# Performance work log

Measured on AMD Instinct MI355X. Metric: run time of the kernel, lower is better.

Reference implementation:

```python
import jax, jax.numpy as jnp
import numpy as np

BATCH, SEQ = 1, 2048
D_MODEL, N_HEADS, D_HEAD = 2048, 16, 128
ROTARY_DIM = 128
N_CTX = 2048
EPS = 1e-5
IGNORE = -100000.0
ATTN_SCALE = float(np.sqrt(D_HEAD))  # use_attn_scale=True, no layer-idx scaling
ROTARY_BASE = 10000.0


def _ln_pre(x):
    # LayerNormPre: center and normalize, no learned scale/bias
    x = x - x.mean(axis=-1, keepdims=True)
    scale = jnp.sqrt((x * x).mean(axis=-1, keepdims=True) + EPS)
    return x / scale


def _sin_cos_rotary(rotary_dim, n_ctx, base=ROTARY_BASE):
    pos = jnp.arange(n_ctx, dtype=jnp.float32)
    dim = jnp.arange(rotary_dim // 2, dtype=jnp.float32)
    freq = base ** (dim / (rotary_dim / 2))
    freq = jnp.repeat(freq, 2)  # einops.repeat 'd -> (d 2)' (interleaved)
    angles = pos[:, None] / freq[None, :]  # [n_ctx, rotary_dim]
    return jnp.sin(angles), jnp.cos(angles)


def _rotate_every_two(x):
    x1 = x[..., 0::2]
    x2 = x[..., 1::2]
    return jnp.stack([-x2, x1], axis=-1).reshape(x.shape)


def _apply_rotary(x, sin, cos):
    # x: [batch, pos, head, d_head]
    n_pos = x.shape[1]
    x_rot = x[..., :ROTARY_DIM]
    x_pass = x[..., ROTARY_DIM:]
    c = cos[:n_pos][:, None, :]  # [pos, 1, rotary_dim] broadcasts over head
    s = sin[:n_pos][:, None, :]
    x_rotated = x_rot * c + _rotate_every_two(x_rot) * s
    return jnp.concatenate([x_rotated, x_pass], axis=-1)


def setup_inputs() -> dict:
    key = jax.random.key(0)
    ks = jax.random.split(key, 6)
    init_std = 0.02
    return {
        "resid_pre": jax.random.normal(ks[0], (BATCH, SEQ, D_MODEL), jnp.float32),
        "W_Q": jax.random.normal(ks[1], (N_HEADS, D_MODEL, D_HEAD), jnp.float32) * init_std,
        "W_K": jax.random.normal(ks[2], (N_HEADS, D_MODEL, D_HEAD), jnp.float32) * init_std,
        "W_V": jax.random.normal(ks[3], (N_HEADS, D_MODEL, D_HEAD), jnp.float32) * init_std,
        "W_O": jax.random.normal(ks[4], (N_HEADS, D_HEAD, D_MODEL), jnp.float32) * init_std,
        "b_Q": jnp.zeros((N_HEADS, D_HEAD), jnp.float32),
        "b_K": jnp.zeros((N_HEADS, D_HEAD), jnp.float32),
        "b_V": jnp.zeros((N_HEADS, D_HEAD), jnp.float32),
        "b_O": jnp.zeros((D_MODEL,), jnp.float32),
    }


def reference(resid_pre, W_Q, W_K, W_V, W_O, b_Q, b_K, b_V, b_O):
    sin, cos = _sin_cos_rotary(ROTARY_DIM, N_CTX)
    xn = _ln_pre(resid_pre)  # LayerNormPre applied to resid_pre for q, k, v
    q = jnp.einsum("bpd,hde->bphe", xn, W_Q) + b_Q
    k = jnp.einsum("bpd,hde->bphe", xn, W_K) + b_K
    v = jnp.einsum("bpd,hde->bphe", xn, W_V) + b_V
    q = _apply_rotary(q, sin, cos)
    k = _apply_rotary(k, sin, cos)
    # attn_scores: [batch, head, query_pos, key_pos]
    scores = jnp.einsum("bqhe,bkhe->bhqk", q, k) / ATTN_SCALE
    n_pos = resid_pre.shape[1]
    causal = jnp.tril(jnp.ones((n_pos, n_pos), dtype=bool))
    scores = jnp.where(causal, scores, jnp.float32(IGNORE))
    attn = jax.nn.softmax(scores, axis=-1)
    z = jnp.einsum("bkhe,bhqk->bqhe", v, attn)
    out = jnp.einsum("bqhe,hed->bqd", z, W_O) + b_O
    return out
```

## Files before the change

### kernel.cpp

```cpp
#include <hip/hip_runtime.h>
#include <hip/hip_bf16.h>

#define SEQ    2048
#define DM     2048
#define NH     16
#define DH     128
#define EPS    1e-5f
#define SCALE_INV 0.08838834764831845f
#define SC2LOG    0.12751744995f

typedef unsigned short u16;
typedef u16  u16x4  __attribute__((ext_vector_type(4)));
typedef u16  u16x8  __attribute__((ext_vector_type(8)));
typedef unsigned u32x4 __attribute__((ext_vector_type(4)));
typedef __bf16 bf16x8 __attribute__((ext_vector_type(8)));
typedef float f32x4 __attribute__((ext_vector_type(4)));

__device__ __forceinline__ u16 f2bf(float f) {
    unsigned int u = __builtin_bit_cast(unsigned int, f);
    u += 0x7fffu + ((u >> 16) & 1u);
    return (u16)(u >> 16);
}
__device__ __forceinline__ float bf2f(u16 v) {
    return __builtin_bit_cast(float, (unsigned)v << 16);
}
__device__ __forceinline__ bf16x8 as_bf(u16x8 v) { return __builtin_bit_cast(bf16x8, v); }

__device__ __forceinline__ void gload16(const u16* g, u16* l) {
    __builtin_amdgcn_global_load_lds(
        (const __attribute__((address_space(1))) unsigned int*)g,
        (__attribute__((address_space(3))) unsigned int*)l, 16, 0, 0);
}

#define VMCNT(N) asm volatile("s_waitcnt vmcnt(" #N ")" ::: "memory")
#define LGKMCNT0 asm volatile("s_waitcnt lgkmcnt(0)" ::: "memory")
#define SCHEDBAR __builtin_amdgcn_sched_barrier(0)
#define BARRIER  __builtin_amdgcn_s_barrier()

__global__ __launch_bounds__(256) void ln_kernel(const float* __restrict__ x,
                                                 u16* __restrict__ xn,
                                                 float2* __restrict__ rope) {
    int row = blockIdx.x, t = threadIdx.x;
    if (t < 64) {
        float freq = powf(10000.f, (float)t * (1.f / 64.f));
        float ang = (float)row / freq;
        rope[row * 64 + t] = make_float2(sinf(ang), cosf(ang));
    }
    const float* xr = x + (size_t)row * DM;
    float4 v0 = *(const float4*)(xr + t * 4);
    float4 v1 = *(const float4*)(xr + 1024 + t * 4);
    float s = v0.x + v0.y + v0.z + v0.w + v1.x + v1.y + v1.z + v1.w;
    float q = v0.x*v0.x + v0.y*v0.y + v0.z*v0.z + v0.w*v0.w
            + v1.x*v1.x + v1.y*v1.y + v1.z*v1.z + v1.w*v1.w;
    #pragma unroll
    for (int o = 32; o; o >>= 1) { s += __shfl_xor(s, o); q += __shfl_xor(q, o); }
    __shared__ float ss[4], qq[4];
    if ((t & 63) == 0) { ss[t >> 6] = s; qq[t >> 6] = q; }
    __syncthreads();
    s = ss[0] + ss[1] + ss[2] + ss[3];
    q = qq[0] + qq[1] + qq[2] + qq[3];
    float mean = s * (1.f / DM);
    float var  = q * (1.f / DM) - mean * mean;
    float rstd = rsqrtf(var + EPS);
    u16* orow = xn + (size_t)row * DM;
    u16x4 o0 = { f2bf((v0.x-mean)*rstd), f2bf((v0.y-mean)*rstd),
                 f2bf((v0.z-mean)*rstd), f2bf((v0.w-mean)*rstd) };
    u16x4 o1 = { f2bf((v1.x-mean)*rstd), f2bf((v1.y-mean)*rstd),
                 f2bf((v1.z-mean)*rstd), f2bf((v1.w-mean)*rstd) };
    *(u16x4*)(orow + t * 4) = o0;
    *(u16x4*)(orow + 1024 + t * 4) = o1;
}

__global__ __launch_bounds__(256) void transpose_all(const float* __restrict__ WQ,
                                                     const float* __restrict__ WK,
                                                     const float* __restrict__ WV,
                                                     const float* __restrict__ WO,
                                                     u16* __restrict__ outW,
                                                     u16* __restrict__ outWO) {
    int z = blockIdx.z;
    const float* in;
    u16* o;
    int r0 = blockIdx.y * 64, c0;
    int inC, outC;
    if (z < 48) {
        int which = z >> 4, h = z & 15;
        in = ((which == 0) ? WQ : (which == 1) ? WK : WV) + (size_t)h * DM * DH;
        o  = outW + (size_t)z * DM * DH;
        c0 = blockIdx.x * 64;
        inC = DH; outC = DM;
    } else {
        in = WO; o = outWO;
        c0 = ((z - 48) * 2 + blockIdx.x) * 64;
        inC = DM; outC = DM;
    }
    __shared__ u16 tile[64][65];
    int t = threadIdx.x;
    #pragma unroll
    for (int it = 0; it < 4; ++it) {
        int idx = t + it * 256;
        int rr = idx >> 4, cc = (idx & 15) * 4;
        float4 v = *(const float4*)(in + (size_t)(r0 + rr) * inC + c0 + cc);
        tile[rr][cc+0] = f2bf(v.x); tile[rr][cc+1] = f2bf(v.y);
        tile[rr][cc+2] = f2bf(v.z); tile[rr][cc+3] = f2bf(v.w);
    }
    __syncthreads();
    #pragma unroll
    for (int it = 0; it < 4; ++it) {
        int idx = t + it * 256;
        int oc = idx >> 4, orr = (idx & 15) * 4;
        u16x4 w = { tile[orr+0][oc], tile[orr+1][oc], tile[orr+2][oc], tile[orr+3][oc] };
        *(u16x4*)(o + (size_t)(c0 + oc) * outC + r0 + orr) = w;
    }
}

__global__ __launch_bounds__(512, 2) void gemm_qkv(const u16* __restrict__ Xn,
                                                   const u16* __restrict__ Wt,
                                                   const float* __restrict__ bQ,
                                                   const float* __restrict__ bK,
                                                   const float* __restrict__ bV,
                                                   const float2* __restrict__ rope,
                                                   u16* __restrict__ qkv) {
    __shared__ u16 As[2][256 * 64], Bs[2][192 * 64];
    int id = blockIdx.x;
    int swz = (id & 7) * 32 + (id >> 3);
    int bx = swz & 7, by = swz >> 3;
    int m0 = bx * 256, n0 = by * 192;

    int t = threadIdx.x, lane = t & 63, wid = t >> 6;
    int wr = wid >> 2, wc = wid & 3;
    int cl = lane & 15, g = lane >> 4;

    auto stage = [&](int buf, int kt) {
        const u16* xa = Xn + (size_t)kt * 64;
        const u16* xb = Wt + (size_t)kt * 64;
        #pragma unroll
        for (int j = 0; j < 4; ++j) {
            int idx = t + j * 512;
            int row = idx >> 3;
            int slotS = (idx & 7) ^ (row & 7);
            gload16(xa + (size_t)(m0 + row) * DM + slotS * 8, &As[buf][idx * 8]);
        }
        #pragma unroll
        for (int j = 0; j < 3; ++j) {
            int idx = t + j * 512;
            int row = idx >> 3;
            int slotS = (idx & 7) ^ (row & 7);
            gload16(xb + (size_t)(n0 + row) * DM + slotS * 8, &Bs[buf][idx * 8]);
        }
    };

    f32x4 acc[8][3] = {};
    stage(0, 0);
    VMCNT(0);
    BARRIER;

    for (int kt = 0; kt < 32; ++kt) {
        int p = kt & 1;
        bool more = (kt + 1 < 32);
        bf16x8 bfr[3][2], af[4][2];
        #pragma unroll
        for (int nj = 0; nj < 3; ++nj)
            #pragma unroll
            for (int kk = 0; kk < 2; ++kk) {
                int row = wc * 48 + nj * 16 + cl;
                int s = (kk * 4 + g) ^ (row & 7);
                bfr[nj][kk] = as_bf(*(const u16x8*)&Bs[p][row * 64 + s * 8]);
            }
        #pragma unroll
        for (int mi = 0; mi < 4; ++mi)
            #pragma unroll
            for (int kk = 0; kk < 2; ++kk) {
                int row = wr * 128 + mi * 16 + cl;
                int s = (kk * 4 + g) ^ (row & 7);
                af[mi][kk] = as_bf(*(const u16x8*)&As[p][row * 64 + s * 8]);
            }
        if (more) stage(p ^ 1, kt + 1);
        __builtin_amdgcn_s_setprio(1);
        #pragma unroll
        for (int mi = 0; mi < 4; ++mi)
            #pragma unroll
            for (int nj = 0; nj < 3; ++nj)
                #pragma unroll
                for (int kk = 0; kk < 2; ++kk)
                    acc[mi][nj] = __builtin_amdgcn_mfma_f32_16x16x32_bf16(af[mi][kk], bfr[nj][kk], acc[mi][nj], 0, 0, 0);
        __builtin_amdgcn_s_setprio(0);
        #pragma unroll
        for (int mi = 0; mi < 4; ++mi)
            #pragma unroll
            for (int kk = 0; kk < 2; ++kk) {
                int row = wr * 128 + 64 + mi * 16 + cl;
                int s = (kk * 4 + g) ^ (row & 7);
                af[mi][kk] = as_bf(*(const u16x8*)&As[p][row * 64 + s * 8]);
            }
        __builtin_amdgcn_s_setprio(1);
        #pragma unroll
        for (int mi = 0; mi < 4; ++mi)
            #pragma unroll
            for (int nj = 0; nj < 3; ++nj)
                #pragma unroll
                for (int kk = 0; kk < 2; ++kk)
                    acc[4 + mi][nj] = __builtin_amdgcn_mfma_f32_16x16x32_bf16(af[mi][kk], bfr[nj][kk], acc[4 + mi][nj], 0, 0, 0);
        __builtin_amdgcn_s_setprio(0);
        VMCNT(0);
        SCHEDBAR;
        BARRIER;
    }

    #pragma unroll
    for (int i = 0; i < 8; ++i)
        #pragma unroll
        for (int nj = 0; nj < 3; ++nj) {
            int eg = n0 + wc * 48 + nj * 16 + cl;
            int which = eg >> 11;
            int h = (eg >> 7) & 15;
            int e = eg & 127;
            const float* bias = (which == 0) ? bQ : (which == 1) ? bK : bV;
            float bb = bias[h * DH + e];
            int p0 = m0 + wr * 128 + i * 16 + g * 4;
            if (which == 2) {
                u16* vbase = qkv + 2ll * NH * SEQ * DH + (size_t)h * DH * SEQ;
                u16x4 o = { f2bf(acc[i][nj][0] + bb), f2bf(acc[i][nj][1] + bb),
                            f2bf(acc[i][nj][2] + bb), f2bf(acc[i][nj][3] + bb) };
                *(u16x4*)(vbase + (size_t)e * SEQ + p0) = o;
            } else {
                u16* outbase = qkv + ((size_t)which * 16 + h) * SEQ * DH;
                #pragma unroll
                for (int r = 0; r < 4; ++r) {
                    int pp = p0 + r;
                    float v = acc[i][nj][r] + bb;
                    float pv = __shfl_xor(v, 1);
                    float2 sc2 = rope[pp * 64 + (e >> 1)];
                    v = (e & 1) ? (v * sc2.y + pv * sc2.x) : (v * sc2.y - pv * sc2.x);
                    outbase[(size_t)pp * DH + e] = f2bf(v);
                }
            }
        }
}

__device__ __forceinline__ int part_prefix(int j) {
    return (j < 16) ? 2 * (j - 8) : (j < 24 ? 16 + 3 * (j - 16) : 40 + 4 * (j - 24));
}

__global__ __launch_bounds__(256) void flash_kernel(const u16* __restrict__ Qg,
                                                    const u16* __restrict__ Kg,
                                                    const u16* __restrict__ Vt,
                                                    u16* __restrict__ Zg,
                                                    u16* __restrict__ pO,
                                                    float2* __restrict__ ml) {
    __shared__ u16 kt[64 * 128];
    __shared__ u16 vt[128 * 64];
    int h = blockIdx.x;
    int rem = blockIdx.y;
    int j = 31, c = 0;
    #pragma unroll 1
    for (int jj = 31; jj >= 0; --jj) {
        int ncj = (jj >> 3) + 1;
        if (rem < ncj) { j = jj; c = rem; break; }
        rem -= ncj;
    }
    int q0 = j * 64;
    int nc = (j >> 3) + 1;
    bool multi = (nc > 1);
    int kt0 = c * 8;
    int kt1 = min(j, c * 8 + 7);

    int t = threadIdx.x, lane = t & 63, w = t >> 6;
    int cl = lane & 15, g = lane >> 4;
    int qw0 = q0 + w * 16;
    const size_t hs = (size_t)h * SEQ;
    int src0 = cl + ((g & 1) << 5);
    int src1 = src0 + 16;
    bool hi = ((g >> 1) & 1) != 0;

    bf16x8 qf[4];
    #pragma unroll
    for (int st = 0; st < 4; ++st)
        qf[st] = as_bf(*(const u16x8*)(Qg + (hs + qw0 + cl) * DH + st * 32 + g * 8));

    f32x4 acc[8] = {};
    float mrun = -3e38f, lsum = 0.f;

    u16x8 kreg[4], vreg[4];
    auto load_tile = [&](int kv0) {
        #pragma unroll
        for (int jj = 0; jj < 4; ++jj) {
            int idx = t + jj * 256;
            kreg[jj] = *(const u16x8*)(Kg + (hs + kv0 + (idx >> 4)) * DH + (idx & 15) * 8);
            vreg[jj] = *(const u16x8*)(Vt + ((size_t)h * DH + (idx >> 3)) * SEQ + kv0 + (idx & 7) * 8);
        }
    };
    auto store_tile = [&]() {
        #pragma unroll
        for (int jj = 0; jj < 4; ++jj) {
            int idx = t + jj * 256;
            int row = idx >> 4, slot = idx & 15;
            *(u16x8*)((char*)kt + row * 256 + ((slot ^ (row & 7)) * 16)) = kreg[jj];
            int e = idx >> 3, ch = idx & 7;
            *(u16x8*)((char*)vt + e * 128 + ((ch ^ (e & 7)) * 16)) = vreg[jj];
        }
    };

    int kvbeg = kt0 * 64, kvend = kt1 * 64;
    load_tile(kvbeg);
    store_tile();

    for (int kv0 = kvbeg; kv0 <= kvend; kv0 += 64) {
        __syncthreads();
        bool more = (kv0 + 64 <= kvend);
        if (more) load_tile(kv0 + 64);

        f32x4 sc[4] = {};
        __builtin_amdgcn_s_setprio(1);
        #pragma unroll
        for (int st = 0; st < 4; ++st)
            #pragma unroll
            for (int cc = 0; cc < 4; ++cc) {
                int row = cc * 16 + cl;
                bf16x8 kf = as_bf(*(const u16x8*)((char*)kt + row * 256 + (((st * 4 + g) ^ (row & 7)) * 16)));
                sc[cc] = __builtin_amdgcn_mfma_f32_16x16x32_bf16(kf, qf[st], sc[cc], 0, 0, 0);
            }
        __builtin_amdgcn_s_setprio(0);

        bool needmask = (kv0 + 63 > qw0);
        int qrow = qw0 + cl;
        float pf[4][4];
        float tm = -3e38f;
        #pragma unroll
        for (int cc = 0; cc < 4; ++cc)
            #pragma unroll
            for (int r = 0; r < 4; ++r) {
                int kvq = kv0 + cc * 16 + g * 4 + r;
                float sval = sc[cc][r] * SC2LOG;
                if (needmask) sval = (kvq <= qrow) ? sval : -3e38f;
                pf[cc][r] = sval;
                tm = fmaxf(tm, sval);
            }
        tm = fmaxf(tm, __shfl_xor(tm, 16));
        tm = fmaxf(tm, __shfl_xor(tm, 32));

        if (!__all(tm <= mrun + 12.f)) {
            float mn = fmaxf(mrun, tm);
            float alpha = exp2f(mrun - mn);
            mrun = mn;
            lsum *= alpha;
            float aR[4];
            #pragma unroll
            for (int r = 0; r < 4; ++r) aR[r] = __shfl(alpha, g * 4 + r);
            #pragma unroll
            for (int n = 0; n < 8; ++n)
                #pragma unroll
                for (int r = 0; r < 4; ++r) acc[n][r] *= aR[r];
        }
        float rs = 0.f;
        #pragma unroll
        for (int cc = 0; cc < 4; ++cc)
            #pragma unroll
            for (int r = 0; r < 4; ++r) {
                float e2 = exp2f(pf[cc][r] - mrun);
                pf[cc][r] = e2;
                rs += e2;
            }
        rs += __shfl_xor(rs, 16);
        rs += __shfl_xor(rs, 32);
        lsum += rs;

        unsigned U[4][2];
        #pragma unroll
        for (int cc = 0; cc < 4; ++cc) {
            asm("v_cvt_pk_bf16_f32 %0, %1, %2" : "=v"(U[cc][0]) : "v"(pf[cc][0]), "v"(pf[cc][1]));
            asm("v_cvt_pk_bf16_f32 %0, %1, %2" : "=v"(U[cc][1]) : "v"(pf[cc][2]), "v"(pf[cc][3]));
        }
        unsigned wv[2][4];
        #pragma unroll
        for (int ks = 0; ks < 2; ++ks)
            #pragma unroll
            for (int hh = 0; hh < 2; ++hh) {
                unsigned e0 = (unsigned)__shfl((int)U[2*ks][hh],   src0);
                unsigned e1 = (unsigned)__shfl((int)U[2*ks][hh],   src1);
                unsigned o0 = (unsigned)__shfl((int)U[2*ks+1][hh], src0);
                unsigned o1 = (unsigned)__shfl((int)U[2*ks+1][hh], src1);
                wv[ks][hh]     = hi ? o0 : e0;
                wv[ks][2 + hh] = hi ? o1 : e1;
            }
        bf16x8 pa[2];
        {
            u32x4 w0 = { wv[0][0], wv[0][1], wv[0][2], wv[0][3] };
            u32x4 w1 = { wv[1][0], wv[1][1], wv[1][2], wv[1][3] };
            pa[0] = __builtin_bit_cast(bf16x8, w0);
            pa[1] = __builtin_bit_cast(bf16x8, w1);
        }

        __builtin_amdgcn_s_setprio(1);
        #pragma unroll
        for (int n = 0; n < 8; ++n)
            #pragma unroll
            for (int ks = 0; ks < 2; ++ks) {
                int e = n * 16 + cl;
                bf16x8 vf = as_bf(*(const u16x8*)((char*)vt + e * 128 + (((ks * 4 + g) ^ (e & 7)) * 16)));
                acc[n] = __builtin_amdgcn_mfma_f32_16x16x32_bf16(pa[ks], vf, acc[n], 0, 0, 0);
            }
        __builtin_amdgcn_s_setprio(0);

        if (!more) break;
        __syncthreads();
        store_tile();
    }

    if (multi) {
        int pidx = h * 72 + part_prefix(j) + c;
        if (lane < 16) ml[(size_t)pidx * 64 + w * 16 + cl] = make_float2(mrun, lsum);
        u16* po = pO + (size_t)pidx * (64 * 128);
        #pragma unroll
        for (int n = 0; n < 8; ++n)
            #pragma unroll
            for (int r = 0; r < 4; ++r)
                po[(w * 16 + g * 4 + r) * 128 + n * 16 + cl] = f2bf(acc[n][r]);
    } else {
        float inv = 1.0f / lsum;
        float invR[4];
        #pragma unroll
        for (int r = 0; r < 4; ++r) invR[r] = __shfl(inv, g * 4 + r);
        #pragma unroll
        for (int n = 0; n < 8; ++n)
            #pragma unroll
            for (int r = 0; r < 4; ++r) {
                int q = qw0 + g * 4 + r;
                Zg[(hs + q) * DH + n * 16 + cl] = f2bf(acc[n][r] * invR[r]);
            }
    }
}

__global__ __launch_bounds__(256) void merge_kernel(const u16* __restrict__ pO,
                                                    const float2* __restrict__ ml,
                                                    u16* __restrict__ Zg) {
    int h = blockIdx.x;
    int j = blockIdx.y + 8;
    int nc = (j >> 3) + 1;
    int pbase = h * 72 + part_prefix(j);
    int t = threadIdx.x;
    int row = t >> 2;
    int c0 = (t & 3) * 32;

    float mv[4], lv[4];
    float M = -3e38f;
    #pragma unroll
    for (int i = 0; i < 4; ++i) {
        int ii = (i < nc) ? i : 0;
        float2 mli = ml[(size_t)(pbase + ii) * 64 + row];
        mv[i] = mli.x; lv[i] = mli.y;
        if (i < nc) M = fmaxf(M, mli.x);
    }
    float wgt[4];
    float L = 0.f;
    #pragma unroll
    for (int i = 0; i < 4; ++i) {
        wgt[i] = (i < nc) ? exp2f(mv[i] - M) : 0.f;
        L += wgt[i] * lv[i];
    }
    float invL = 1.f / L;

    #pragma unroll
    for (int ccc = 0; ccc < 32; ccc += 8) {
        float o[8] = {};
        #pragma unroll
        for (int i = 0; i < 4; ++i) {
            int ii = (i < nc) ? i : 0;
            u16x8 v = *(const u16x8*)(pO + ((size_t)(pbase + ii) * 64 + row) * 128 + c0 + ccc);
            #pragma unroll
            for (int k = 0; k < 8; ++k) o[k] += wgt[i] * bf2f(v[k]);
        }
        u16x8 zv;
        #pragma unroll
        for (int k = 0; k < 8; ++k) zv[k] = f2bf(o[k] * invL);
        *(u16x8*)(Zg + ((size_t)h * SEQ + j * 64 + row) * DH + c0 + ccc) = zv;
    }
}

__global__ __launch_bounds__(256, 2) void gemm_out(const u16* __restrict__ Z,
                                                   const u16* __restrict__ Wot,
                                                   const float* __restrict__ bO,
                                                   float* __restrict__ out) {
    __shared__ u16 As[2][128 * 64], Bs[2][128 * 64];
    int id = blockIdx.x;
    int swz = (id & 7) * 32 + (id >> 3);
    int m0 = (swz & 15) * 128, n0 = (swz >> 4) * 128;
    int t = threadIdx.x, lane = t & 63, w = t >> 6;
    int wr = w >> 1, wc = w & 1;
    int cl = lane & 15, g = lane >> 4;

    auto stage = [&](int buf, int kt) {
        int k0 = kt * 64;
        int hh = k0 >> 7, e0 = k0 & 127;
        #pragma unroll
        for (int j = 0; j < 4; ++j) {
            int idx = t + j * 256;
            int row = idx >> 3;
            int slotS = (idx & 7) ^ (row & 7);
            gload16(Z + ((size_t)hh * SEQ + m0 + row) * DH + e0 + slotS * 8, &As[buf][idx * 8]);
            gload16(Wot + (size_t)(n0 + row) * DM + k0 + slotS * 8, &Bs[buf][idx * 8]);
        }
    };

    f32x4 acc[4][4] = {};
    stage(0, 0);
    VMCNT(0);
    BARRIER;
    for (int kt = 0; kt < 32; ++kt) {
        int p = kt & 1;
        bool more = (kt + 1 < 32);
        bf16x8 af[4][2], bfr[4][2];
        #pragma unroll
        for (int i = 0; i < 4; ++i)
            #pragma unroll
            for (int kk = 0; kk < 2; ++kk) {
                int rowA = wr * 64 + i * 16 + cl;
                af[i][kk] = as_bf(*(const u16x8*)&As[p][rowA * 64 + (((kk * 4 + g) ^ (rowA & 7)) * 8)]);
                int rowB = wc * 64 + i * 16 + cl;
                bfr[i][kk] = as_bf(*(const u16x8*)&Bs[p][rowB * 64 + (((kk * 4 + g) ^ (rowB & 7)) * 8)]);
            }
        if (more) stage(p ^ 1, kt + 1);
        __builtin_amdgcn_s_setprio(1);
        #pragma unroll
        for (int i = 0; i < 4; ++i)
            #pragma unroll
            for (int j = 0; j < 4; ++j)
                #pragma unroll
                for (int kk = 0; kk < 2; ++kk)
                    acc[i][j] = __builtin_amdgcn_mfma_f32_16x16x32_bf16(af[i][kk], bfr[j][kk], acc[i][j], 0, 0, 0);
        __builtin_amdgcn_s_setprio(0);
        VMCNT(0);
        SCHEDBAR;
        BARRIER;
    }
    #pragma unroll
    for (int i = 0; i < 4; ++i)
        #pragma unroll
        for (int j = 0; j < 4; ++j) {
            int col = n0 + wc * 64 + j * 16 + cl;
            float bb = bO[col];
            #pragma unroll
            for (int r = 0; r < 4; ++r) {
                int p = m0 + wr * 64 + i * 16 + g * 4 + r;
                out[(size_t)p * DM + col] = acc[i][j][r] + bb;
            }
        }
}

extern "C" void kernel_launch(void* const* d_in, const int* in_sizes, int n_in,
                              void* d_out, int out_size, void* d_ws, size_t ws_size,
                              hipStream_t stream) {
    const float* resid = (const float*)d_in[0];
    const float* WQ = (const float*)d_in[1];
    const float* WK = (const float*)d_in[2];
    const float* WV = (const float*)d_in[3];
    const float* WO = (const float*)d_in[4];
    const float* bQ = (const float*)d_in[5];
    const float* bK = (const float*)d_in[6];
    const float* bV = (const float*)d_in[7];
    const float* bO = (const float*)d_in[8];
    float* out = (float*)d_out;
    char* ws = (char*)d_ws;

    float2* rope = (float2*)(ws);
    u16* xn   = (u16*)(ws + (1ll  << 20));
    u16* Wt   = (u16*)(ws + (9ll  << 20));
    u16* Wot  = (u16*)(ws + (33ll << 20));
    u16* qkv  = (u16*)(ws + (41ll << 20));
    u16* z    = (u16*)(ws + (65ll << 20));
    u16* pO   = (u16*)(ws);
    float2* ml = (float2*)(ws + (20ll << 20));

    ln_kernel<<<SEQ, 256, 0, stream>>>(resid, xn, rope);

    transpose_all<<<dim3(2, 32, 64), 256, 0, stream>>>(WQ, WK, WV, WO, Wt, Wot);

    gemm_qkv<<<256, 512, 0, stream>>>(xn, Wt, bQ, bK, bV, rope, qkv);

    const u16* Qg = qkv;
    const u16* Kg = qkv + 1ll * NH * SEQ * DH;
    const u16* Vt = qkv + 2ll * NH * SEQ * DH;
    flash_kernel<<<dim3(NH, 80), 256, 0, stream>>>(Qg, Kg, Vt, z, pO, ml);
    merge_kernel<<<dim3(NH, 24), 256, 0, stream>>>(pO, ml, z);

    gemm_out<<<256, 256, 0, stream>>>(z, Wot, bO, out);
}
```

Baseline: 178.6 us.

## Load K and V fragments directly from global memory in flash kernel

Removes the shared-memory staging of K and V tiles, along with the register prefetch and both block barriers. Each wave now reads its MFMA operand fragments straight from global memory (relying on L1/L2) instead of cooperatively loading and swizzling tiles into LDS. This removes synchronisation and LDS traffic. In exchange, the four waves in a block each fetch the same K/V data redundantly and the loads are no longer prefetched ahead of compute, so memory latency may be exposed.

```diff
diff --git a/kernel.cpp b/kernel.cpp
--- a/kernel.cpp
+++ b/kernel.cpp
@@ -247,8 +247,6 @@
                                                     u16* __restrict__ Zg,
                                                     u16* __restrict__ pO,
                                                     float2* __restrict__ ml) {
-    __shared__ u16 kt[64 * 128];
-    __shared__ u16 vt[128 * 64];
     int h = blockIdx.x;
     int rem = blockIdx.y;
     int j = 31, c = 0;
@@ -272,6 +270,9 @@
     int src1 = src0 + 16;
     bool hi = ((g >> 1) & 1) != 0;
 
+    const u16* kp = Kg + (hs + cl) * DH + g * 8;
+    const u16* vp = Vt + ((size_t)h * DH + cl) * SEQ + g * 8;
+
     bf16x8 qf[4];
     #pragma unroll
     for (int st = 0; st < 4; ++st)
@@ -280,43 +281,16 @@
     f32x4 acc[8] = {};
     float mrun = -3e38f, lsum = 0.f;
 
-    u16x8 kreg[4], vreg[4];
-    auto load_tile = [&](int kv0) {
-        #pragma unroll
-        for (int jj = 0; jj < 4; ++jj) {
-            int idx = t + jj * 256;
-            kreg[jj] = *(const u16x8*)(Kg + (hs + kv0 + (idx >> 4)) * DH + (idx & 15) * 8);
-            vreg[jj] = *(const u16x8*)(Vt + ((size_t)h * DH + (idx >> 3)) * SEQ + kv0 + (idx & 7) * 8);
-        }
-    };
-    auto store_tile = [&]() {
-        #pragma unroll
-        for (int jj = 0; jj < 4; ++jj) {
-            int idx = t + jj * 256;
-            int row = idx >> 4, slot = idx & 15;
-            *(u16x8*)((char*)kt + row * 256 + ((slot ^ (row & 7)) * 16)) = kreg[jj];
-            int e = idx >> 3, ch = idx & 7;
-            *(u16x8*)((char*)vt + e * 128 + ((ch ^ (e & 7)) * 16)) = vreg[jj];
-        }
-    };
-
     int kvbeg = kt0 * 64, kvend = kt1 * 64;
-    load_tile(kvbeg);
-    store_tile();
 
     for (int kv0 = kvbeg; kv0 <= kvend; kv0 += 64) {
-        __syncthreads();
-        bool more = (kv0 + 64 <= kvend);
-        if (more) load_tile(kv0 + 64);
-
         f32x4 sc[4] = {};
         __builtin_amdgcn_s_setprio(1);
         #pragma unroll
         for (int st = 0; st < 4; ++st)
             #pragma unroll
             for (int cc = 0; cc < 4; ++cc) {
-                int row = cc * 16 + cl;
-                bf16x8 kf = as_bf(*(const u16x8*)((char*)kt + row * 256 + (((st * 4 + g) ^ (row & 7)) * 16)));
+                bf16x8 kf = as_bf(*(const u16x8*)(kp + (size_t)(kv0 + cc * 16) * DH + st * 32));
                 sc[cc] = __builtin_amdgcn_mfma_f32_16x16x32_bf16(kf, qf[st], sc[cc], 0, 0, 0);
             }
         __builtin_amdgcn_s_setprio(0);
@@ -395,15 +369,10 @@
         for (int n = 0; n < 8; ++n)
             #pragma unroll
             for (int ks = 0; ks < 2; ++ks) {
-                int e = n * 16 + cl;
-                bf16x8 vf = as_bf(*(const u16x8*)((char*)vt + e * 128 + (((ks * 4 + g) ^ (e & 7)) * 16)));
+                bf16x8 vf = as_bf(*(const u16x8*)(vp + (size_t)(n * 16) * SEQ + kv0 + ks * 32));
                 acc[n] = __builtin_amdgcn_mfma_f32_16x16x32_bf16(pa[ks], vf, acc[n], 0, 0, 0);
             }
         __builtin_amdgcn_s_setprio(0);
-
-        if (!more) break;
-        __syncthreads();
-        store_tile();
     }
 
     if (multi) {
```

Result: slower. 284.5 us (+59.3%).

## Process two 64-row query blocks per flash workgroup to reuse K/V tiles

Applied to the files above, without the earlier changes.

Each flash-attention workgroup now handles 128 query rows, two 16-row strips per wave, against the same shared-memory K/V tiles. This halves the global loads and LDS staging per query row and gives each wave twice the MFMA work between barriers. The partition bookkeeping and the merge kernel are rescaled to match. In exchange the grid shrinks from 1280 to 640 workgroups, register pressure roughly doubles, and more masked work is done on diagonal tiles.

```diff
diff --git a/kernel.cpp b/kernel.cpp
--- a/kernel.cpp
+++ b/kernel.cpp
@@ -238,7 +238,7 @@
 }
 
 __device__ __forceinline__ int part_prefix(int j) {
-    return (j < 16) ? 2 * (j - 8) : (j < 24 ? 16 + 3 * (j - 16) : 40 + 4 * (j - 24));
+    return (j < 8) ? 2 * (j - 4) : (j < 12 ? 8 + 3 * (j - 8) : 20 + 4 * (j - 12));
 }
 
 __global__ __launch_bounds__(256) void flash_kernel(const u16* __restrict__ Qg,
@@ -251,34 +251,38 @@
     __shared__ u16 vt[128 * 64];
     int h = blockIdx.x;
     int rem = blockIdx.y;
-    int j = 31, c = 0;
+    int j = 15, c = 0;
     #pragma unroll 1
-    for (int jj = 31; jj >= 0; --jj) {
-        int ncj = (jj >> 3) + 1;
+    for (int jj = 15; jj >= 0; --jj) {
+        int ncj = (jj >> 2) + 1;
         if (rem < ncj) { j = jj; c = rem; break; }
         rem -= ncj;
     }
-    int q0 = j * 64;
-    int nc = (j >> 3) + 1;
+    int q0 = j * 128;
+    int nc = (j >> 2) + 1;
     bool multi = (nc > 1);
     int kt0 = c * 8;
-    int kt1 = min(j, c * 8 + 7);
+    int kt1 = min(2 * j + 1, c * 8 + 7);
 
     int t = threadIdx.x, lane = t & 63, w = t >> 6;
     int cl = lane & 15, g = lane >> 4;
-    int qw0 = q0 + w * 16;
+    int qs0 = q0 + w * 16;
+    int qs1 = qs0 + 64;
     const size_t hs = (size_t)h * SEQ;
     int src0 = cl + ((g & 1) << 5);
     int src1 = src0 + 16;
     bool hi = ((g >> 1) & 1) != 0;
 
-    bf16x8 qf[4];
-    #pragma unroll
-    for (int st = 0; st < 4; ++st)
-        qf[st] = as_bf(*(const u16x8*)(Qg + (hs + qw0 + cl) * DH + st * 32 + g * 8));
-
-    f32x4 acc[8] = {};
-    float mrun = -3e38f, lsum = 0.f;
+    bf16x8 qf0[4], qf1[4];
+    #pragma unroll
+    for (int st = 0; st < 4; ++st) {
+        qf0[st] = as_bf(*(const u16x8*)(Qg + (hs + qs0 + cl) * DH + st * 32 + g * 8));
+        qf1[st] = as_bf(*(const u16x8*)(Qg + (hs + qs1 + cl) * DH + st * 32 + g * 8));
+    }
+
+    f32x4 acc0[8] = {}, acc1[8] = {};
+    float mrun0 = -3e38f, lsum0 = 0.f;
+    float mrun1 = -3e38f, lsum1 = 0.f;
 
     u16x8 kreg[4], vreg[4];
     auto load_tile = [&](int kv0) {
@@ -309,7 +313,7 @@
         bool more = (kv0 + 64 <= kvend);
         if (more) load_tile(kv0 + 64);
 
-        f32x4 sc[4] = {};
+        f32x4 sc0[4] = {}, sc1[4] = {};
         __builtin_amdgcn_s_setprio(1);
         #pragma unroll
         for (int st = 0; st < 4; ++st)
@@ -317,78 +321,82 @@
             for (int cc = 0; cc < 4; ++cc) {
                 int row = cc * 16 + cl;
                 bf16x8 kf = as_bf(*(const u16x8*)((char*)kt + row * 256 + (((st * 4 + g) ^ (row & 7)) * 16)));
-                sc[cc] = __builtin_amdgcn_mfma_f32_16x16x32_bf16(kf, qf[st], sc[cc], 0, 0, 0);
+                sc0[cc] = __builtin_amdgcn_mfma_f32_16x16x32_bf16(kf, qf0[st], sc0[cc], 0, 0, 0);
+                sc1[cc] = __builtin_amdgcn_mfma_f32_16x16x32_bf16(kf, qf1[st], sc1[cc], 0, 0, 0);
             }
         __builtin_amdgcn_s_setprio(0);
 
-        bool needmask = (kv0 + 63 > qw0);
-        int qrow = qw0 + cl;
-        float pf[4][4];
-        float tm = -3e38f;
-        #pragma unroll
-        for (int cc = 0; cc < 4; ++cc)
-            #pragma unroll
-            for (int r = 0; r < 4; ++r) {
-                int kvq = kv0 + cc * 16 + g * 4 + r;
-                float sval = sc[cc][r] * SC2LOG;
-                if (needmask) sval = (kvq <= qrow) ? sval : -3e38f;
-                pf[cc][r] = sval;
-                tm = fmaxf(tm, sval);
-            }
-        tm = fmaxf(tm, __shfl_xor(tm, 16));
-        tm = fmaxf(tm, __shfl_xor(tm, 32));
-
-        if (!__all(tm <= mrun + 12.f)) {
-            float mn = fmaxf(mrun, tm);
-            float alpha = exp2f(mrun - mn);
-            mrun = mn;
-            lsum *= alpha;
-            float aR[4];
-            #pragma unroll
-            for (int r = 0; r < 4; ++r) aR[r] = __shfl(alpha, g * 4 + r);
-            #pragma unroll
-            for (int n = 0; n < 8; ++n)
-                #pragma unroll
-                for (int r = 0; r < 4; ++r) acc[n][r] *= aR[r];
-        }
-        float rs = 0.f;
-        #pragma unroll
-        for (int cc = 0; cc < 4; ++cc)
-            #pragma unroll
-            for (int r = 0; r < 4; ++r) {
-                float e2 = exp2f(pf[cc][r] - mrun);
-                pf[cc][r] = e2;
-                rs += e2;
-            }
-        rs += __shfl_xor(rs, 16);
-        rs += __shfl_xor(rs, 32);
-        lsum += rs;
-
-        unsigned U[4][2];
-        #pragma unroll
-        for (int cc = 0; cc < 4; ++cc) {
-            asm("v_cvt_pk_bf16_f32 %0, %1, %2" : "=v"(U[cc][0]) : "v"(pf[cc][0]), "v"(pf[cc][1]));
-            asm("v_cvt_pk_bf16_f32 %0, %1, %2" : "=v"(U[cc][1]) : "v"(pf[cc][2]), "v"(pf[cc][3]));
-        }
-        unsigned wv[2][4];
-        #pragma unroll
-        for (int ks = 0; ks < 2; ++ks)
-            #pragma unroll
-            for (int hh = 0; hh < 2; ++hh) {
-                unsigned e0 = (unsigned)__shfl((int)U[2*ks][hh],   src0);
-                unsigned e1 = (unsigned)__shfl((int)U[2*ks][hh],   src1);
-                unsigned o0 = (unsigned)__shfl((int)U[2*ks+1][hh], src0);
-                unsigned o1 = (unsigned)__shfl((int)U[2*ks+1][hh], src1);
-                wv[ks][hh]     = hi ? o0 : e0;
-                wv[ks][2 + hh] = hi ? o1 : e1;
-            }
-        bf16x8 pa[2];
-        {
+        bf16x8 pa0[2], pa1[2];
+        auto smT = [&](f32x4 (&sc)[4], int qb, float& mrun, float& lsum,
+                       f32x4 (&acc)[8], bf16x8 (&pa)[2]) {
+            bool needmask = (kv0 + 63 > qb);
+            int qrow = qb + cl;
+            float pf[4][4];
+            float tm = -3e38f;
+            #pragma unroll
+            for (int cc = 0; cc < 4; ++cc)
+                #pragma unroll
+                for (int r = 0; r < 4; ++r) {
+                    int kvq = kv0 + cc * 16 + g * 4 + r;
+                    float sval = sc[cc][r] * SC2LOG;
+                    if (needmask) sval = (kvq <= qrow) ? sval : -3e38f;
+                    pf[cc][r] = sval;
+                    tm = fmaxf(tm, sval);
+                }
+            tm = fmaxf(tm, __shfl_xor(tm, 16));
+            tm = fmaxf(tm, __shfl_xor(tm, 32));
+
+            if (!__all(tm <= mrun + 12.f)) {
+                float mn = fmaxf(mrun, tm);
+                float alpha = exp2f(mrun - mn);
+                mrun = mn;
+                lsum *= alpha;
+                float aR[4];
+                #pragma unroll
+                for (int r = 0; r < 4; ++r) aR[r] = __shfl(alpha, g * 4 + r);
+                #pragma unroll
+                for (int n = 0; n < 8; ++n)
+                    #pragma unroll
+                    for (int r = 0; r < 4; ++r) acc[n][r] *= aR[r];
+            }
+            float rs = 0.f;
+            #pragma unroll
+            for (int cc = 0; cc < 4; ++cc)
+                #pragma unroll
+                for (int r = 0; r < 4; ++r) {
+                    float e2 = exp2f(pf[cc][r] - mrun);
+                    pf[cc][r] = e2;
+                    rs += e2;
+                }
+            rs += __shfl_xor(rs, 16);
+            rs += __shfl_xor(rs, 32);
+            lsum += rs;
+
+            unsigned U[4][2];
+            #pragma unroll
+            for (int cc = 0; cc < 4; ++cc) {
+                asm("v_cvt_pk_bf16_f32 %0, %1, %2" : "=v"(U[cc][0]) : "v"(pf[cc][0]), "v"(pf[cc][1]));
+                asm("v_cvt_pk_bf16_f32 %0, %1, %2" : "=v"(U[cc][1]) : "v"(pf[cc][2]), "v"(pf[cc][3]));
+            }
+            unsigned wv[2][4];
+            #pragma unroll
+            for (int ks = 0; ks < 2; ++ks)
+                #pragma unroll
+                for (int hh = 0; hh < 2; ++hh) {
+                    unsigned e0 = (unsigned)__shfl((int)U[2*ks][hh],   src0);
+                    unsigned e1 = (unsigned)__shfl((int)U[2*ks][hh],   src1);
+                    unsigned o0 = (unsigned)__shfl((int)U[2*ks+1][hh], src0);
+                    unsigned o1 = (unsigned)__shfl((int)U[2*ks+1][hh], src1);
+                    wv[ks][hh]     = hi ? o0 : e0;
+                    wv[ks][2 + hh] = hi ? o1 : e1;
+                }
             u32x4 w0 = { wv[0][0], wv[0][1], wv[0][2], wv[0][3] };
             u32x4 w1 = { wv[1][0], wv[1][1], wv[1][2], wv[1][3] };
             pa[0] = __builtin_bit_cast(bf16x8, w0);
             pa[1] = __builtin_bit_cast(bf16x8, w1);
-        }
+        };
+        smT(sc0, qs0, mrun0, lsum0, acc0, pa0);
+        smT(sc1, qs1, mrun1, lsum1, acc1, pa1);
 
         __builtin_amdgcn_s_setprio(1);
         #pragma unroll
@@ -397,7 +405,8 @@
             for (int ks = 0; ks < 2; ++ks) {
                 int e = n * 16 + cl;
                 bf16x8 vf = as_bf(*(const u16x8*)((char*)vt + e * 128 + (((ks * 4 + g) ^ (e & 7)) * 16)));
-                acc[n] = __builtin_amdgcn_mfma_f32_16x16x32_bf16(pa[ks], vf, acc[n], 0, 0, 0);
+                acc0[n] = __builtin_amdgcn_mfma_f32_16x16x32_bf16(pa0[ks], vf, acc0[n], 0, 0, 0);
+                acc1[n] = __builtin_amdgcn_mfma_f32_16x16x32_bf16(pa1[ks], vf, acc1[n], 0, 0, 0);
             }
         __builtin_amdgcn_s_setprio(0);
 
@@ -407,25 +416,33 @@
     }
 
     if (multi) {
-        int pidx = h * 72 + part_prefix(j) + c;
-        if (lane < 16) ml[(size_t)pidx * 64 + w * 16 + cl] = make_float2(mrun, lsum);
-        u16* po = pO + (size_t)pidx * (64 * 128);
+        int pidx = h * 36 + part_prefix(j) + c;
+        if (lane < 16) {
+            ml[(size_t)pidx * 128 + w * 16 + cl]      = make_float2(mrun0, lsum0);
+            ml[(size_t)pidx * 128 + 64 + w * 16 + cl] = make_float2(mrun1, lsum1);
+        }
+        u16* po = pO + (size_t)pidx * (128 * 128);
         #pragma unroll
         for (int n = 0; n < 8; ++n)
             #pragma unroll
-            for (int r = 0; r < 4; ++r)
-                po[(w * 16 + g * 4 + r) * 128 + n * 16 + cl] = f2bf(acc[n][r]);
+            for (int r = 0; r < 4; ++r) {
+                po[(w * 16 + g * 4 + r) * 128 + n * 16 + cl]        = f2bf(acc0[n][r]);
+                po[(64 + w * 16 + g * 4 + r) * 128 + n * 16 + cl]   = f2bf(acc1[n][r]);
+            }
     } else {
-        float inv = 1.0f / lsum;
-        float invR[4];
-        #pragma unroll
-        for (int r = 0; r < 4; ++r) invR[r] = __shfl(inv, g * 4 + r);
+        float inv0 = 1.0f / lsum0, inv1 = 1.0f / lsum1;
+        float invR0[4], invR1[4];
+        #pragma unroll
+        for (int r = 0; r < 4; ++r) {
+            invR0[r] = __shfl(inv0, g * 4 + r);
+            invR1[r] = __shfl(inv1, g * 4 + r);
+        }
         #pragma unroll
         for (int n = 0; n < 8; ++n)
             #pragma unroll
             for (int r = 0; r < 4; ++r) {
-                int q = qw0 + g * 4 + r;
-                Zg[(hs + q) * DH + n * 16 + cl] = f2bf(acc[n][r] * invR[r]);
+                Zg[(hs + qs0 + g * 4 + r) * DH + n * 16 + cl] = f2bf(acc0[n][r] * invR0[r]);
+                Zg[(hs + qs1 + g * 4 + r) * DH + n * 16 + cl] = f2bf(acc1[n][r] * invR1[r]);
             }
     }
 }
@@ -434,19 +451,19 @@
                                                     const float2* __restrict__ ml,
                                                     u16* __restrict__ Zg) {
     int h = blockIdx.x;
-    int j = blockIdx.y + 8;
-    int nc = (j >> 3) + 1;
-    int pbase = h * 72 + part_prefix(j);
+    int j = blockIdx.y + 4;
+    int nc = (j >> 2) + 1;
+    int pbase = h * 36 + part_prefix(j);
     int t = threadIdx.x;
-    int row = t >> 2;
-    int c0 = (t & 3) * 32;
+    int row = t >> 1;
+    int c0 = (t & 1) * 64;
 
     float mv[4], lv[4];
     float M = -3e38f;
     #pragma unroll
     for (int i = 0; i < 4; ++i) {
         int ii = (i < nc) ? i : 0;
-        float2 mli = ml[(size_t)(pbase + ii) * 64 + row];
+        float2 mli = ml[(size_t)(pbase + ii) * 128 + row];
         mv[i] = mli.x; lv[i] = mli.y;
         if (i < nc) M = fmaxf(M, mli.x);
     }
@@ -460,19 +477,19 @@
     float invL = 1.f / L;
 
     #pragma unroll
-    for (int ccc = 0; ccc < 32; ccc += 8) {
+    for (int ccc = 0; ccc < 64; ccc += 8) {
         float o[8] = {};
         #pragma unroll
         for (int i = 0; i < 4; ++i) {
             int ii = (i < nc) ? i : 0;
-            u16x8 v = *(const u16x8*)(pO + ((size_t)(pbase + ii) * 64 + row) * 128 + c0 + ccc);
+            u16x8 v = *(const u16x8*)(pO + ((size_t)(pbase + ii) * 128 + row) * 128 + c0 + ccc);
             #pragma unroll
             for (int k = 0; k < 8; ++k) o[k] += wgt[i] * bf2f(v[k]);
         }
         u16x8 zv;
         #pragma unroll
         for (int k = 0; k < 8; ++k) zv[k] = f2bf(o[k] * invL);
-        *(u16x8*)(Zg + ((size_t)h * SEQ + j * 64 + row) * DH + c0 + ccc) = zv;
+        *(u16x8*)(Zg + ((size_t)h * SEQ + j * 128 + row) * DH + c0 + ccc) = zv;
     }
 }
 
@@ -579,8 +596,8 @@
     const u16* Qg = qkv;
     const u16* Kg = qkv + 1ll * NH * SEQ * DH;
     const u16* Vt = qkv + 2ll * NH * SEQ * DH;
-    flash_kernel<<<dim3(NH, 80), 256, 0, stream>>>(Qg, Kg, Vt, z, pO, ml);
-    merge_kernel<<<dim3(NH, 24), 256, 0, stream>>>(pO, ml, z);
+    flash_kernel<<<dim3(NH, 40), 256, 0, stream>>>(Qg, Kg, Vt, z, pO, ml);
+    merge_kernel<<<dim3(NH, 12), 256, 0, stream>>>(pO, ml, z);
 
     gemm_out<<<256, 256, 0, stream>>>(z, Wot, bO, out);
 }
```

Result: slower. 203.8 us (+14.1%).
